# Optimization experiments

Measured on AMD Instinct MI355X. Metric: run time of the kernel, lower is better.

## Reference

```python
import jax, jax.numpy as jnp
import numpy as np
from jax.ops import segment_sum

N_NODES = 50000
N_EDGES = 800000
IN_FEATS = 128
H_FEATS = 256
NUM_CLASSES = 16


def setup_inputs() -> dict:
    key = jax.random.key(0)
    k1, k2, k3, k4, k5 = jax.random.split(key, 5)
    in_feat = jax.random.normal(k1, (N_NODES, IN_FEATS), dtype=jnp.float32)
    src = jax.random.randint(k2, (N_EDGES,), 0, N_NODES, dtype=jnp.int32)
    dst = jax.random.randint(k3, (N_EDGES,), 0, N_NODES, dtype=jnp.int32)
    # Glorot-ish scaled params
    W_gc = jax.random.normal(k4, (IN_FEATS, H_FEATS), dtype=jnp.float32) / np.sqrt(IN_FEATS)
    b_gc = jnp.zeros((H_FEATS,), dtype=jnp.float32)
    W_fc = jax.random.normal(k5, (H_FEATS, NUM_CLASSES), dtype=jnp.float32) / np.sqrt(H_FEATS)
    b_fc = jnp.zeros((NUM_CLASSES,), dtype=jnp.float32)
    return {"in_feat": in_feat, "src": src, "dst": dst,
            "W_gc": W_gc, "b_gc": b_gc, "W_fc": W_fc, "b_fc": b_fc}


def reference(in_feat, src, dst, W_gc, b_gc, W_fc, b_fc):
    n = in_feat.shape[0]
    ones = jnp.ones_like(src, dtype=in_feat.dtype)
    # DGL GraphConv, norm='both': D_out^{-1/2} on source side, sum-aggregate,
    # D_in^{-1/2} on destination side. Degrees clamped to >= 1.
    deg_out = jnp.clip(segment_sum(ones, src, num_segments=n), 1.0)
    deg_in = jnp.clip(segment_sum(ones, dst, num_segments=n), 1.0)
    x = in_feat * jax.lax.rsqrt(deg_out)[:, None]            # [N, in]
    agg = segment_sum(x[src], dst, num_segments=n)           # [N, in] irregular gather+scatter
    agg = agg * jax.lax.rsqrt(deg_in)[:, None]
    # in_feats <= h_feats -> aggregate first, then project (DGL ordering)
    h = agg @ W_gc + b_gc                                    # [N, h]
    h = jax.nn.relu(h)
    logits = h @ W_fc + b_fc                                 # [N, num_classes]
    return jax.nn.sigmoid(logits)
```

## Files before the change

kernel.cpp:

```cpp
#include <hip/hip_runtime.h>
#include <hip/hip_bf16.h>

#define IN_F  128
#define H_F   256
#define NC    16
#define BM    64
#define CAP   64
#define PCAP  8192

typedef short bf16x8 __attribute__((ext_vector_type(8)));
typedef float f32x4  __attribute__((ext_vector_type(4)));

__device__ __forceinline__ unsigned short f2bf(float x) {
    union { float f; unsigned u; } v; v.f = x;
    unsigned r = v.u + 0x7FFF + ((v.u >> 16) & 1);
    return (unsigned short)(r >> 16);
}
__device__ __forceinline__ float bflo(unsigned x) {
    union { unsigned u; float f; } v; v.u = x << 16; return v.f;
}
__device__ __forceinline__ float bfhi(unsigned x) {
    union { unsigned u; float f; } v; v.u = x & 0xffff0000u; return v.f;
}

__global__ __launch_bounds__(256) void gcn_part(
    const int* __restrict__ src, const int* __restrict__ dst,
    int* __restrict__ curS, int* __restrict__ curD,
    unsigned short* __restrict__ srcP, unsigned* __restrict__ dstP,
    const float* __restrict__ W_gc, const float* __restrict__ W_fc,
    unsigned short* __restrict__ Wp, unsigned short* __restrict__ Wfp,
    const float* __restrict__ in_feat, unsigned* __restrict__ xb,
    int n_edges, int n_feat4, int nb_edge, int np) {
    __shared__ int cS[256], cD[256];
    int b0 = blockIdx.x, tid = threadIdx.x;
    if (b0 < nb_edge) {
        unsigned sv[16], dv[16];
        int ebase = b0 * 4096;
        #pragma unroll
        for (int r = 0; r < 16; ++r) {
            int e = ebase + r * 256 + tid;
            if (e < n_edges) { sv[r] = (unsigned)src[e]; dv[r] = (unsigned)dst[e]; }
            else { sv[r] = 0xFFFFFFFFu; dv[r] = 0xFFFFFFFFu; }
        }
        cS[tid] = 0; cD[tid] = 0;
        __syncthreads();
        #pragma unroll
        for (int r = 0; r < 16; ++r) {
            if (dv[r] != 0xFFFFFFFFu) {
                atomicAdd(&cS[sv[r] >> 8], 1);
                atomicAdd(&cD[dv[r] >> 8], 1);
            }
        }
        __syncthreads();
        if (tid < np) {
            int c = cS[tid];
            cS[tid] = c ? atomicAdd(&curS[tid], c) : 0;
            c = cD[tid];
            cD[tid] = c ? atomicAdd(&curD[tid], c) : 0;
        }
        __syncthreads();
        #pragma unroll
        for (int r = 0; r < 16; ++r) {
            if (dv[r] != 0xFFFFFFFFu) {
                unsigned s = sv[r], d = dv[r];
                int ps = atomicAdd(&cS[s >> 8], 1);
                if (ps < PCAP) srcP[(size_t)(s >> 8) * PCAP + ps] = (unsigned short)s;
                int pd = atomicAdd(&cD[d >> 8], 1);
                if (pd < PCAP) dstP[(size_t)(d >> 8) * PCAP + pd] =
                    ((d & 255u) << 16) | (s & 0xffffu);
            }
        }
        return;
    }
    int b = b0 - nb_edge;
    if (b < 128) {
        int g = b * 256 + tid;
        {
            int j = g & 7, l = (g >> 3) & 63, t = g >> 9;
            int kt = t & 3, ct = t >> 2;
            int k = kt * 32 + ((l >> 4) << 3) + j;
            int col = ct * 16 + (l & 15);
            Wp[g] = f2bf(W_gc[k * 256 + col]);
        }
        if (g < 4096) {
            int j = g & 7, l = (g >> 3) & 63, kt = g >> 9;
            int k = kt * 32 + ((l >> 4) << 3) + j;
            Wfp[g] = f2bf(W_fc[k * 16 + (l & 15)]);
        }
        return;
    }
    int idx = (b - 128) * 256 + tid;
    if (idx < n_feat4) {
        float4 v = ((const float4*)in_feat)[idx];
        uint2 o;
        o.x = (unsigned)f2bf(v.x) | ((unsigned)f2bf(v.y) << 16);
        o.y = (unsigned)f2bf(v.z) | ((unsigned)f2bf(v.w) << 16);
        ((uint2*)xb)[idx] = o;
    }
}

__global__ __launch_bounds__(256) void gcn_bucket(
    const unsigned short* __restrict__ srcP, const unsigned* __restrict__ dstP,
    const int* __restrict__ curS, const int* __restrict__ curD,
    float* __restrict__ rsq, int* __restrict__ cnt_in,
    unsigned short* __restrict__ esrc, int n, int np) {
    __shared__ unsigned hist[256];
    __shared__ unsigned short bucket[256 * CAP];
    int p = blockIdx.x, tid = threadIdx.x;
    hist[tid] = 0;
    __syncthreads();
    if (p < np) {
        int cnt = curS[p]; if (cnt > PCAP) cnt = PCAP;
        const unsigned short* sp = srcP + (size_t)p * PCAP;
        for (int i = tid; i < cnt; i += 256)
            atomicAdd(&hist[sp[i] & 255], 1);
        __syncthreads();
        int node = p * 256 + tid;
        if (node < n) rsq[node] = rsqrtf(fmaxf((float)hist[tid], 1.0f));
    } else {
        int pp = p - np;
        int cnt = curD[pp]; if (cnt > PCAP) cnt = PCAP;
        const unsigned* dp = dstP + (size_t)pp * PCAP;
        for (int i = tid; i < cnt; i += 256) {
            unsigned pair = dp[i];
            unsigned dl = pair >> 16;
            unsigned pos = atomicAdd(&hist[dl], 1);
            if (pos < CAP) bucket[(dl << 6) + pos] = (unsigned short)(pair & 0xffffu);
        }
        __syncthreads();
        unsigned* eb = (unsigned*)(esrc + ((size_t)pp << 14));
        const unsigned* bu = (const unsigned*)bucket;
        int maxrow = n - pp * 256;
        int words = (maxrow >= 256) ? 8192 : (maxrow > 0 ? maxrow * 32 : 0);
        for (int i = tid; i < words; i += 256) eb[i] = bu[i];
        int node = pp * 256 + tid;
        if (node < n) cnt_in[node] = (int)hist[tid];
    }
}

__global__ __launch_bounds__(256) void gcn_aggregate(
    const unsigned* __restrict__ xb, const unsigned short* __restrict__ esrc,
    const int* __restrict__ cnt_in, const float* __restrict__ rsq,
    unsigned* __restrict__ aggb, int n) {
    int wave = (blockIdx.x * blockDim.x + threadIdx.x) >> 6;
    int lane = threadIdx.x & 63;
    if (wave >= n) return;
    int wv = __builtin_amdgcn_readfirstlane(wave);
    int cnt = cnt_in[wv];
    if (cnt > CAP) cnt = CAP;
    const unsigned short* es = esrc + ((size_t)wv << 6);
    float ax[8], ay[8];
    #pragma unroll
    for (int u = 0; u < 8; ++u) { ax[u] = 0.f; ay[u] = 0.f; }
    int nfull = cnt & ~7;
    int i = 0;
    for (; i < nfull; i += 8) {
        uint4 sp = *(const uint4*)(es + i);
        int s0 = sp.x & 0xffff, s1 = sp.x >> 16;
        int s2 = sp.y & 0xffff, s3 = sp.y >> 16;
        int s4 = sp.z & 0xffff, s5 = sp.z >> 16;
        int s6 = sp.w & 0xffff, s7 = sp.w >> 16;
        float r0 = rsq[s0];
        float r1 = rsq[s1];
        float r2 = rsq[s2];
        float r3 = rsq[s3];
        float r4 = rsq[s4];
        float r5 = rsq[s5];
        float r6 = rsq[s6];
        float r7 = rsq[s7];
        unsigned v0 = xb[(size_t)s0 * 64 + lane];
        unsigned v1 = xb[(size_t)s1 * 64 + lane];
        unsigned v2 = xb[(size_t)s2 * 64 + lane];
        unsigned v3 = xb[(size_t)s3 * 64 + lane];
        unsigned v4 = xb[(size_t)s4 * 64 + lane];
        unsigned v5 = xb[(size_t)s5 * 64 + lane];
        unsigned v6 = xb[(size_t)s6 * 64 + lane];
        unsigned v7 = xb[(size_t)s7 * 64 + lane];
        ax[0] = fmaf(bflo(v0), r0, ax[0]); ay[0] = fmaf(bfhi(v0), r0, ay[0]);
        ax[1] = fmaf(bflo(v1), r1, ax[1]); ay[1] = fmaf(bfhi(v1), r1, ay[1]);
        ax[2] = fmaf(bflo(v2), r2, ax[2]); ay[2] = fmaf(bfhi(v2), r2, ay[2]);
        ax[3] = fmaf(bflo(v3), r3, ax[3]); ay[3] = fmaf(bfhi(v3), r3, ay[3]);
        ax[4] = fmaf(bflo(v4), r4, ax[4]); ay[4] = fmaf(bfhi(v4), r4, ay[4]);
        ax[5] = fmaf(bflo(v5), r5, ax[5]); ay[5] = fmaf(bfhi(v5), r5, ay[5]);
        ax[6] = fmaf(bflo(v6), r6, ax[6]); ay[6] = fmaf(bfhi(v6), r6, ay[6]);
        ax[7] = fmaf(bflo(v7), r7, ax[7]); ay[7] = fmaf(bfhi(v7), r7, ay[7]);
    }
    if (i < cnt) {
        uint4 sp = *(const uint4*)(es + i);
        int t0 = sp.x & 0xffff, t1 = sp.x >> 16;
        int t2 = sp.y & 0xffff, t3 = sp.y >> 16;
        int t4 = sp.z & 0xffff, t5 = sp.z >> 16;
        int t6 = sp.w & 0xffff, t7 = sp.w >> 16;
        int rem = cnt - i;
        int s0 = (0 < rem) ? t0 : 0, s1 = (1 < rem) ? t1 : 0;
        int s2 = (2 < rem) ? t2 : 0, s3 = (3 < rem) ? t3 : 0;
        int s4 = (4 < rem) ? t4 : 0, s5 = (5 < rem) ? t5 : 0;
        int s6 = (6 < rem) ? t6 : 0, s7 = (7 < rem) ? t7 : 0;
        float r0 = (0 < rem) ? rsq[s0] : 0.f;
        float r1 = (1 < rem) ? rsq[s1] : 0.f;
        float r2 = (2 < rem) ? rsq[s2] : 0.f;
        float r3 = (3 < rem) ? rsq[s3] : 0.f;
        float r4 = (4 < rem) ? rsq[s4] : 0.f;
        float r5 = (5 < rem) ? rsq[s5] : 0.f;
        float r6 = (6 < rem) ? rsq[s6] : 0.f;
        float r7 = (7 < rem) ? rsq[s7] : 0.f;
        unsigned v0 = xb[(size_t)s0 * 64 + lane];
        unsigned v1 = xb[(size_t)s1 * 64 + lane];
        unsigned v2 = xb[(size_t)s2 * 64 + lane];
        unsigned v3 = xb[(size_t)s3 * 64 + lane];
        unsigned v4 = xb[(size_t)s4 * 64 + lane];
        unsigned v5 = xb[(size_t)s5 * 64 + lane];
        unsigned v6 = xb[(size_t)s6 * 64 + lane];
        unsigned v7 = xb[(size_t)s7 * 64 + lane];
        ax[0] = fmaf(bflo(v0), r0, ax[0]); ay[0] = fmaf(bfhi(v0), r0, ay[0]);
        ax[1] = fmaf(bflo(v1), r1, ax[1]); ay[1] = fmaf(bfhi(v1), r1, ay[1]);
        ax[2] = fmaf(bflo(v2), r2, ax[2]); ay[2] = fmaf(bfhi(v2), r2, ay[2]);
        ax[3] = fmaf(bflo(v3), r3, ax[3]); ay[3] = fmaf(bfhi(v3), r3, ay[3]);
        ax[4] = fmaf(bflo(v4), r4, ax[4]); ay[4] = fmaf(bfhi(v4), r4, ay[4]);
        ax[5] = fmaf(bflo(v5), r5, ax[5]); ay[5] = fmaf(bfhi(v5), r5, ay[5]);
        ax[6] = fmaf(bflo(v6), r6, ax[6]); ay[6] = fmaf(bfhi(v6), r6, ay[6]);
        ax[7] = fmaf(bflo(v7), r7, ax[7]); ay[7] = fmaf(bfhi(v7), r7, ay[7]);
    }
    float axs = ((ax[0] + ax[1]) + (ax[2] + ax[3])) + ((ax[4] + ax[5]) + (ax[6] + ax[7]));
    float ays = ((ay[0] + ay[1]) + (ay[2] + ay[3])) + ((ay[4] + ay[5]) + (ay[6] + ay[7]));
    float ri = rsqrtf(fmaxf((float)cnt, 1.0f));
    aggb[(size_t)wv * 64 + lane] =
        (unsigned)f2bf(axs * ri) | ((unsigned)f2bf(ays * ri) << 16);
}

__global__ __launch_bounds__(256) void gcn_mlp(
    const unsigned* __restrict__ aggb, const unsigned short* __restrict__ Wp,
    const unsigned short* __restrict__ Wfp, const float* __restrict__ b_gc,
    const float* __restrict__ b_fc, float* __restrict__ out, int n) {
    extern __shared__ char smraw[];
    unsigned short* Wfl = (unsigned short*)smraw;
    unsigned short* Al  = Wfl + 4096;
    unsigned short* Hl  = Al + 8192;
    float* bgl = (float*)(Hl + 16384);
    float* bfl = bgl + 256;

    int tid = threadIdx.x;
    int lane = tid & 63, w = tid >> 6;

    for (int i = tid; i < 512; i += 256) ((float4*)Wfl)[i] = ((const float4*)Wfp)[i];
    bgl[tid] = b_gc[tid];
    if (tid < NC) bfl[tid] = b_fc[tid];

    const bf16x8* WpB = (const bf16x8*)Wp;
    int ntiles = (n + BM - 1) / BM;
    for (int tile = blockIdx.x; tile < ntiles; tile += gridDim.x) {
        __syncthreads();
        int row0 = tile * BM;
        for (int i = tid; i < 1024; i += 256) {
            int r = i >> 4, cb = i & 15;
            int node = row0 + r;
            float4 v = (node < n) ? ((const float4*)aggb)[(size_t)node * 16 + cb]
                                  : make_float4(0.f, 0.f, 0.f, 0.f);
            ((float4*)Al)[r * 16 + (cb ^ (r & 7))] = v;
        }
        __syncthreads();

        bf16x8 af[4];
        {
            int r = lane & 15;
            #pragma unroll
            for (int kt = 0; kt < 4; ++kt) {
                int cb = kt * 4 + (lane >> 4);
                af[kt] = *((const bf16x8*)Al + ((w * 16 + r) * 16 + (cb ^ (r & 7))));
            }
        }
        f32x4 acc[16];
        #pragma unroll
        for (int ct = 0; ct < 16; ++ct) {
            acc[ct] = (f32x4){0.f, 0.f, 0.f, 0.f};
            #pragma unroll
            for (int kt = 0; kt < 4; ++kt) {
                bf16x8 bfr = WpB[(ct * 4 + kt) * 64 + lane];
                acc[ct] = __builtin_amdgcn_mfma_f32_16x16x32_bf16(af[kt], bfr, acc[ct], 0, 0, 0);
            }
        }
        #pragma unroll
        for (int ct = 0; ct < 16; ++ct) {
            int col = ct * 16 + (lane & 15);
            float bv = bgl[col];
            #pragma unroll
            for (int r4 = 0; r4 < 4; ++r4) {
                int r = ((lane >> 4) << 2) + r4;
                float hv = fmaxf(acc[ct][r4] + bv, 0.f);
                int cu = col >> 3;
                Hl[(w * 16 + r) * 256 + ((cu ^ (r & 7)) << 3) + (col & 7)] = f2bf(hv);
            }
        }
        f32x4 acc2 = (f32x4){0.f, 0.f, 0.f, 0.f};
        {
            int r = lane & 15;
            #pragma unroll
            for (int kt = 0; kt < 8; ++kt) {
                int cu = kt * 4 + (lane >> 4);
                bf16x8 a2 = *((const bf16x8*)Hl + ((w * 16 + r) * 32 + (cu ^ (r & 7))));
                bf16x8 b2 = *((const bf16x8*)Wfl + (kt * 64 + lane));
                acc2 = __builtin_amdgcn_mfma_f32_16x16x32_bf16(a2, b2, acc2, 0, 0, 0);
            }
        }
        int col = lane & 15;
        float bv = bfl[col];
        #pragma unroll
        for (int r4 = 0; r4 < 4; ++r4) {
            int row = row0 + w * 16 + ((lane >> 4) << 2) + r4;
            if (row < n) {
                float v = acc2[r4] + bv;
                out[(size_t)row * NC + col] = 1.f / (1.f + expf(-v));
            }
        }
    }
}

extern "C" void kernel_launch(void* const* d_in, const int* in_sizes, int n_in,
                              void* d_out, int out_size, void* d_ws, size_t ws_size,
                              hipStream_t stream) {
    const float* in_feat = (const float*)d_in[0];
    const int*   src     = (const int*)d_in[1];
    const int*   dst     = (const int*)d_in[2];
    const float* W_gc    = (const float*)d_in[3];
    const float* b_gc    = (const float*)d_in[4];
    const float* W_fc    = (const float*)d_in[5];
    const float* b_fc    = (const float*)d_in[6];
    float* out = (float*)d_out;

    int n_nodes = in_sizes[0] / IN_F;
    int n_edges = in_sizes[1];
    int np = (n_nodes + 255) >> 8;

    int* curS = (int*)d_ws;
    int* curD = curS + 256;
    float* rsq = (float*)(curD + 256);
    int* cnt_in  = (int*)(rsq + n_nodes);
    unsigned short* srcP = (unsigned short*)(cnt_in + n_nodes);
    unsigned* dstP = (unsigned*)(srcP + (size_t)np * PCAP);
    unsigned short* esrc = (unsigned short*)(dstP + (size_t)np * PCAP);
    unsigned short* Wp   = esrc + (size_t)np * 256 * CAP;
    unsigned short* Wfp  = Wp + 32768;
    unsigned* xb   = (unsigned*)(Wfp + 4096);
    unsigned* aggb = xb + (size_t)n_nodes * 64;

    hipMemsetAsync(d_ws, 0, 512 * sizeof(int), stream);

    {
        int n_feat4 = n_nodes * 32;
        int nb_edge = (n_edges + 4095) / 4096;
        int nb_conv = (n_feat4 + 255) / 256;
        gcn_part<<<nb_edge + 128 + nb_conv, 256, 0, stream>>>(
            src, dst, curS, curD, srcP, dstP, W_gc, W_fc, Wp, Wfp,
            in_feat, xb, n_edges, n_feat4, nb_edge, np);
    }
    gcn_bucket<<<2 * np, 256, 0, stream>>>(srcP, dstP, curS, curD,
                                           rsq, cnt_in, esrc, n_nodes, np);
    {
        int blocks = (n_nodes + 3) / 4;
        gcn_aggregate<<<blocks, 256, 0, stream>>>(xb, esrc, cnt_in, rsq, aggb, n_nodes);
    }
    {
        size_t smem = (size_t)(4096 + 8192 + 16384) * 2 + 1024 + 64;
        hipFuncSetAttribute((const void*)gcn_mlp,
                            hipFuncAttributeMaxDynamicSharedMemorySize, (int)smem);
        gcn_mlp<<<512, 256, smem, stream>>>(aggb, Wp, Wfp, b_gc, b_fc, out, n_nodes);
    }
}
```

Measured before the change: 86.82 us.

## Pad edge buckets with zero-weight dummy node and size MLP grid to tiles

Adds a sentinel node (index n) whose bf16 features and rsqrt-degree are zero. Every destination bucket is prefilled with this sentinel, so the aggregate loop can run whole groups of 8 edges with no masked tail block. This removes the divergent, predicated remainder code in the gather kernel. In exchange the bucket kernel clears shared memory and adds a barrier, and tail groups now issue dummy loads to one row. The MLP launch also changes from a fixed 512 blocks to one block per 64-row tile.

Result: slower. 100.7 us (+16.0%).

```diff
diff --git a/kernel.cpp b/kernel.cpp
--- a/kernel.cpp
+++ b/kernel.cpp
@@ -30,7 +30,7 @@
     const float* __restrict__ W_gc, const float* __restrict__ W_fc,
     unsigned short* __restrict__ Wp, unsigned short* __restrict__ Wfp,
     const float* __restrict__ in_feat, unsigned* __restrict__ xb,
-    int n_edges, int n_feat4, int nb_edge, int np) {
+    int n_edges, int n_feat4, int nb_edge, int np, int n_nodes) {
     __shared__ int cS[256], cD[256];
     int b0 = blockIdx.x, tid = threadIdx.x;
     if (b0 < nb_edge) {
@@ -97,6 +97,8 @@
         o.y = (unsigned)f2bf(v.z) | ((unsigned)f2bf(v.w) << 16);
         ((uint2*)xb)[idx] = o;
     }
+    if (idx < 32)
+        ((uint2*)xb)[(size_t)n_nodes * 32 + idx] = make_uint2(0u, 0u);
 }
 
 __global__ __launch_bounds__(256) void gcn_bucket(
@@ -117,10 +119,15 @@
         __syncthreads();
         int node = p * 256 + tid;
         if (node < n) rsq[node] = rsqrtf(fmaxf((float)hist[tid], 1.0f));
+        else if (node == n) rsq[node] = 0.f;
     } else {
         int pp = p - np;
+        unsigned dummy2 = ((unsigned)n & 0xffffu) | (((unsigned)n & 0xffffu) << 16);
+        unsigned* bu32 = (unsigned*)bucket;
+        for (int i = tid; i < 8192; i += 256) bu32[i] = dummy2;
         int cnt = curD[pp]; if (cnt > PCAP) cnt = PCAP;
         const unsigned* dp = dstP + (size_t)pp * PCAP;
+        __syncthreads();
         for (int i = tid; i < cnt; i += 256) {
             unsigned pair = dp[i];
             unsigned dl = pair >> 16;
@@ -152,9 +159,7 @@
     float ax[8], ay[8];
     #pragma unroll
     for (int u = 0; u < 8; ++u) { ax[u] = 0.f; ay[u] = 0.f; }
-    int nfull = cnt & ~7;
-    int i = 0;
-    for (; i < nfull; i += 8) {
+    for (int i = 0; i < cnt; i += 8) {
         uint4 sp = *(const uint4*)(es + i);
         int s0 = sp.x & 0xffff, s1 = sp.x >> 16;
         int s2 = sp.y & 0xffff, s3 = sp.y >> 16;
@@ -185,42 +190,6 @@
         ax[6] = fmaf(bflo(v6), r6, ax[6]); ay[6] = fmaf(bfhi(v6), r6, ay[6]);
         ax[7] = fmaf(bflo(v7), r7, ax[7]); ay[7] = fmaf(bfhi(v7), r7, ay[7]);
     }
-    if (i < cnt) {
-        uint4 sp = *(const uint4*)(es + i);
-        int t0 = sp.x & 0xffff, t1 = sp.x >> 16;
-        int t2 = sp.y & 0xffff, t3 = sp.y >> 16;
-        int t4 = sp.z & 0xffff, t5 = sp.z >> 16;
-        int t6 = sp.w & 0xffff, t7 = sp.w >> 16;
-        int rem = cnt - i;
-        int s0 = (0 < rem) ? t0 : 0, s1 = (1 < rem) ? t1 : 0;
-        int s2 = (2 < rem) ? t2 : 0, s3 = (3 < rem) ? t3 : 0;
-        int s4 = (4 < rem) ? t4 : 0, s5 = (5 < rem) ? t5 : 0;
-        int s6 = (6 < rem) ? t6 : 0, s7 = (7 < rem) ? t7 : 0;
-        float r0 = (0 < rem) ? rsq[s0] : 0.f;
-        float r1 = (1 < rem) ? rsq[s1] : 0.f;
-        float r2 = (2 < rem) ? rsq[s2] : 0.f;
-        float r3 = (3 < rem) ? rsq[s3] : 0.f;
-        float r4 = (4 < rem) ? rsq[s4] : 0.f;
-        float r5 = (5 < rem) ? rsq[s5] : 0.f;
-        float r6 = (6 < rem) ? rsq[s6] : 0.f;
-        float r7 = (7 < rem) ? rsq[s7] : 0.f;
-        unsigned v0 = xb[(size_t)s0 * 64 + lane];
-        unsigned v1 = xb[(size_t)s1 * 64 + lane];
-        unsigned v2 = xb[(size_t)s2 * 64 + lane];
-        unsigned v3 = xb[(size_t)s3 * 64 + lane];
-        unsigned v4 = xb[(size_t)s4 * 64 + lane];
-        unsigned v5 = xb[(size_t)s5 * 64 + lane];
-        unsigned v6 = xb[(size_t)s6 * 64 + lane];
-        unsigned v7 = xb[(size_t)s7 * 64 + lane];
-        ax[0] = fmaf(bflo(v0), r0, ax[0]); ay[0] = fmaf(bfhi(v0), r0, ay[0]);
-        ax[1] = fmaf(bflo(v1), r1, ax[1]); ay[1] = fmaf(bfhi(v1), r1, ay[1]);
-        ax[2] = fmaf(bflo(v2), r2, ax[2]); ay[2] = fmaf(bfhi(v2), r2, ay[2]);
-        ax[3] = fmaf(bflo(v3), r3, ax[3]); ay[3] = fmaf(bfhi(v3), r3, ay[3]);
-        ax[4] = fmaf(bflo(v4), r4, ax[4]); ay[4] = fmaf(bfhi(v4), r4, ay[4]);
-        ax[5] = fmaf(bflo(v5), r5, ax[5]); ay[5] = fmaf(bfhi(v5), r5, ay[5]);
-        ax[6] = fmaf(bflo(v6), r6, ax[6]); ay[6] = fmaf(bfhi(v6), r6, ay[6]);
-        ax[7] = fmaf(bflo(v7), r7, ax[7]); ay[7] = fmaf(bfhi(v7), r7, ay[7]);
-    }
     float axs = ((ax[0] + ax[1]) + (ax[2] + ax[3])) + ((ax[4] + ax[5]) + (ax[6] + ax[7]));
     float ays = ((ay[0] + ay[1]) + (ay[2] + ay[3])) + ((ay[4] + ay[5]) + (ay[6] + ay[7]));
     float ri = rsqrtf(fmaxf((float)cnt, 1.0f));
@@ -330,18 +299,19 @@
     int n_nodes = in_sizes[0] / IN_F;
     int n_edges = in_sizes[1];
     int np = (n_nodes + 255) >> 8;
+    int rsq_slots = (n_nodes + 1 + 3) & ~3;
 
     int* curS = (int*)d_ws;
     int* curD = curS + 256;
     float* rsq = (float*)(curD + 256);
-    int* cnt_in  = (int*)(rsq + n_nodes);
+    int* cnt_in  = (int*)(rsq + rsq_slots);
     unsigned short* srcP = (unsigned short*)(cnt_in + n_nodes);
     unsigned* dstP = (unsigned*)(srcP + (size_t)np * PCAP);
     unsigned short* esrc = (unsigned short*)(dstP + (size_t)np * PCAP);
     unsigned short* Wp   = esrc + (size_t)np * 256 * CAP;
     unsigned short* Wfp  = Wp + 32768;
     unsigned* xb   = (unsigned*)(Wfp + 4096);
-    unsigned* aggb = xb + (size_t)n_nodes * 64;
+    unsigned* aggb = xb + (size_t)(n_nodes + 1) * 64;
 
     hipMemsetAsync(d_ws, 0, 512 * sizeof(int), stream);
 
@@ -351,7 +321,7 @@
         int nb_conv = (n_feat4 + 255) / 256;
         gcn_part<<<nb_edge + 128 + nb_conv, 256, 0, stream>>>(
             src, dst, curS, curD, srcP, dstP, W_gc, W_fc, Wp, Wfp,
-            in_feat, xb, n_edges, n_feat4, nb_edge, np);
+            in_feat, xb, n_edges, n_feat4, nb_edge, np, n_nodes);
     }
     gcn_bucket<<<2 * np, 256, 0, stream>>>(srcP, dstP, curS, curD,
                                            rsq, cnt_in, esrc, n_nodes, np);
@@ -363,6 +333,7 @@
         size_t smem = (size_t)(4096 + 8192 + 16384) * 2 + 1024 + 64;
         hipFuncSetAttribute((const void*)gcn_mlp,
                             hipFuncAttributeMaxDynamicSharedMemorySize, (int)smem);
-        gcn_mlp<<<512, 256, smem, stream>>>(aggb, Wp, Wfp, b_gc, b_fc, out, n_nodes);
-    }
-}
+        int ntiles = (n_nodes + BM - 1) / BM;
+        gcn_mlp<<<ntiles, 256, smem, stream>>>(aggb, Wp, Wfp, b_gc, b_fc, out, n_nodes);
+    }
+}
```
